# Optimization experiments

Measured on AMD Instinct MI355X. Metric: run time of the kernel, lower is better.

## Reference

```python
import jax, jax.numpy as jnp
import numpy as np

NUM_HEADS = 16
MASKED_BIAS = -10000.0


def setup_inputs() -> dict:
    key = jax.random.key(0)
    ks = jax.random.split(key, 5)
    B, S, D = 4, 2048, 1024
    return {
        "encodings": jax.random.normal(ks[0], (B, S, D), dtype=jnp.float32),
        "w_attn": jax.random.normal(ks[1], (D, 3 * D), dtype=jnp.float32) * (1.0 / np.sqrt(D)),
        "b_attn": jax.random.normal(ks[2], (3 * D,), dtype=jnp.float32) * 0.02,
        "w_proj": jax.random.normal(ks[3], (D, D), dtype=jnp.float32) * (1.0 / np.sqrt(D)),
        "b_proj": jax.random.normal(ks[4], (D,), dtype=jnp.float32) * 0.02,
    }


def reference(encodings, w_attn, b_attn, w_proj, b_proj):
    B, S, D = encodings.shape
    H = NUM_HEADS
    hs = D // H
    qkv = encodings @ w_attn + b_attn            # [B,S,3D]
    q, k, v = jnp.split(qkv, 3, axis=-1)
    # 'b s (h c) -> b h s c'
    def split_heads(x):
        return x.reshape(B, S, H, hs).transpose(0, 2, 1, 3)
    q, k, v = split_heads(q), split_heads(k), split_heads(v)
    # scores[b,h,f,t] = q[t] . k[f] / sqrt(hs)  (f=key, t=query)
    scores = jnp.einsum('bhtc,bhfc->bhft', q, k) / np.sqrt(hs).astype(jnp.float32)
    # causal: query t may attend key f iff t >= f  -> upper-tri in (f,t)
    causal = jnp.triu(jnp.ones((S, S), dtype=bool))  # [f,t]
    scores = jnp.where(causal[None, None], scores, jnp.asarray(MASKED_BIAS, scores.dtype))
    attn = jax.nn.softmax(scores, axis=-2)       # softmax over keys (f)
    ctx = jnp.einsum('bhft,bhfc->bhtc', attn, v)  # [B,H,S,hs]
    ctx = ctx.transpose(0, 2, 1, 3).reshape(B, S, D)  # 'b h s c -> b s (h c)'
    return ctx @ w_proj + b_proj
```

## Files before the change

kernel.cpp:

```cpp
#include <hip/hip_runtime.h>
#include <hip/hip_bf16.h>
#include <stdint.h>

#define NH  16
#define SEQ 2048
#define DM  1024
#define HS  64
#define NB  4

typedef __attribute__((ext_vector_type(8))) short bf16x8;
typedef __attribute__((ext_vector_type(4))) float f32x4;

__device__ __forceinline__ unsigned short f2b(float f) {
    unsigned int u = __float_as_uint(f);
    u += 0x7fffu + ((u >> 16) & 1u);
    return (unsigned short)(u >> 16);
}

__device__ __forceinline__ void gload16(const void* g, void* lds) {
    __builtin_amdgcn_global_load_lds(
        (const __attribute__((address_space(1))) unsigned int*)g,
        (__attribute__((address_space(3))) unsigned int*)lds,
        16, 0, 0);
}

__global__ void k_cvt(const float* __restrict__ in, unsigned short* __restrict__ out, int n) {
    int i = (blockIdx.x * blockDim.x + threadIdx.x) * 4;
    if (i >= n) return;
    float4 v = *(const float4*)(in + i);
    ushort4 o;
    o.x = f2b(v.x); o.y = f2b(v.y); o.z = f2b(v.z); o.w = f2b(v.w);
    *(ushort4*)(out + i) = o;
}

__global__ void k_tr(const float* __restrict__ in, unsigned short* __restrict__ out, int K, int N) {
    __shared__ float t[32][33];
    int n0 = blockIdx.x * 32, k0 = blockIdx.y * 32;
    int tx = threadIdx.x, ty = threadIdx.y;
#pragma unroll
    for (int j = 0; j < 32; j += 8)
        t[ty + j][tx] = in[(size_t)(k0 + ty + j) * N + n0 + tx];
    __syncthreads();
#pragma unroll
    for (int j = 0; j < 32; j += 8)
        out[(size_t)(n0 + ty + j) * K + k0 + tx] = f2b(t[tx][ty + j]);
}

template <int MODE>
__global__ __launch_bounds__(256, 2) void k_gemm(
    const unsigned short* __restrict__ A,
    const unsigned short* __restrict__ Bt,
    const float* __restrict__ bias,
    void* __restrict__ outp, int M, int N, int K)
{
    __shared__ unsigned short As[128 * 64];
    __shared__ unsigned short Bs[128 * 64];
    const int tid = threadIdx.x;
    const int l = tid & 63, w = tid >> 6;
    const int lg = l >> 4, li = l & 15;
    const int m0 = blockIdx.x * 128, n0 = blockIdx.y * 128;
    const int wm = (w >> 1) * 64, wn = (w & 1) * 64;

    f32x4 acc[4][4] = {};

    for (int k0 = 0; k0 < K; k0 += 64) {
#pragma unroll
        for (int i = 0; i < 4; i++) {
            int ch = i * 256 + tid;
            int row = ch >> 3, cc = ch & 7;
            int sc = cc ^ (row & 7);
            gload16(A + (size_t)(m0 + row) * K + k0 + sc * 8, &As[(i * 256 + w * 64) * 8]);
        }
#pragma unroll
        for (int i = 0; i < 4; i++) {
            int ch = i * 256 + tid;
            int row = ch >> 3, cc = ch & 7;
            int sc = cc ^ (row & 7);
            gload16(Bt + (size_t)(n0 + row) * K + k0 + sc * 8, &Bs[(i * 256 + w * 64) * 8]);
        }
        __syncthreads();
#pragma unroll
        for (int kc = 0; kc < 2; kc++) {
            bf16x8 af[4], bfr[4];
#pragma unroll
            for (int mi = 0; mi < 4; mi++) {
                int row = wm + mi * 16 + li;
                int chunk = (kc * 4 + lg) ^ (row & 7);
                af[mi] = *(const bf16x8*)&As[row * 64 + chunk * 8];
            }
#pragma unroll
            for (int ni = 0; ni < 4; ni++) {
                int row = wn + ni * 16 + li;
                int chunk = (kc * 4 + lg) ^ (row & 7);
                bfr[ni] = *(const bf16x8*)&Bs[row * 64 + chunk * 8];
            }
#pragma unroll
            for (int mi = 0; mi < 4; mi++)
#pragma unroll
                for (int ni = 0; ni < 4; ni++)
                    acc[mi][ni] = __builtin_amdgcn_mfma_f32_16x16x32_bf16(af[mi], bfr[ni], acc[mi][ni], 0, 0, 0);
        }
        __syncthreads();
    }

#pragma unroll
    for (int mi = 0; mi < 4; mi++) {
        int mrow = m0 + wm + mi * 16 + lg * 4;
#pragma unroll
        for (int ni = 0; ni < 4; ni++) {
            int col = n0 + wn + ni * 16 + li;
            float bv = bias[col];
            if (MODE == 0) {
                float* out = (float*)outp;
#pragma unroll
                for (int r = 0; r < 4; r++)
                    out[(size_t)(mrow + r) * N + col] = acc[mi][ni][r] + bv;
            } else {
                unsigned short* out = (unsigned short*)outp;
                const size_t QKV1 = (size_t)NB * NH * SEQ * HS;
                int sqkv = col >> 10;
                int d = col & 1023;
                int h = d >> 6, c = d & 63;
                float scale = (sqkv == 0) ? 0.18033688f : 1.0f;
#pragma unroll
                for (int r = 0; r < 4; r++) {
                    int m = mrow + r;
                    int bq = m >> 11, sp = m & 2047;
                    size_t off;
                    if (sqkv == 2)
                        off = 2 * QKV1 + ((size_t)(bq * NH + h) * HS + c) * SEQ + sp;
                    else
                        off = (size_t)sqkv * QKV1 + ((size_t)(bq * NH + h) * SEQ + sp) * HS + c;
                    out[off] = f2b((acc[mi][ni][r] + bv) * scale);
                }
            }
        }
    }
}

__global__ __launch_bounds__(256, 2) void k_attn(
    const unsigned short* __restrict__ qkv,
    unsigned short* __restrict__ ctx)
{
    __shared__ unsigned short Ks[2][64 * 64];
    __shared__ unsigned short Vts[2][64 * 64];
    __shared__ unsigned short Ps[4 * 32 * 64];
    const int tid = threadIdx.x;
    const int l = tid & 63, w = tid >> 6;
    const int lg = l >> 4, li = l & 15;
    const int bh = blockIdx.x;
    const int qa = blockIdx.y;
    const int qb = 15 - qa;
    const int qA0 = qa * 128, qB0 = qb * 128;
    const int na = qA0 / 64 + 2, nbt = qB0 / 64 + 2;
    const size_t hb = (size_t)bh * SEQ * HS;
    const size_t QKV1 = (size_t)NB * NH * SEQ * HS;
    const unsigned short* Qg = qkv + hb;
    const unsigned short* Kg = qkv + QKV1 + hb;
    const unsigned short* VTg = qkv + 2 * QKV1 + hb;

    bf16x8 aqA[2][2], aqB[2][2];
#pragma unroll
    for (int rt = 0; rt < 2; rt++) {
        int tA = qA0 + rt * 64 + w * 16 + li;
        aqA[rt][0] = *(const bf16x8*)(Qg + (size_t)tA * HS + lg * 8);
        aqA[rt][1] = *(const bf16x8*)(Qg + (size_t)tA * HS + 32 + lg * 8);
        int tB = qB0 + rt * 64 + w * 16 + li;
        aqB[rt][0] = *(const bf16x8*)(Qg + (size_t)tB * HS + lg * 8);
        aqB[rt][1] = *(const bf16x8*)(Qg + (size_t)tB * HS + 32 + lg * 8);
    }

    f32x4 accA[2][4] = {}, accB[2][4] = {};
    float mrA[2][4], lsA[2][4], mrB[2][4], lsB[2][4];
#pragma unroll
    for (int rt = 0; rt < 2; rt++)
#pragma unroll
        for (int r = 0; r < 4; r++) {
            mrA[rt][r] = -1e30f; lsA[rt][r] = 0.f;
            mrB[rt][r] = -1e30f; lsB[rt][r] = 0.f;
        }

    auto stage = [&](int buf, int f0) {
#pragma unroll
        for (int i = 0; i < 2; i++) {
            int ch = i * 256 + tid;
            int row = ch >> 3, cc = ch & 7;
            int sc = cc ^ (row & 7);
            gload16(Kg + (size_t)(f0 + row) * HS + sc * 8, &Ks[buf][(i * 256 + w * 64) * 8]);
        }
#pragma unroll
        for (int i = 0; i < 2; i++) {
            int ch = i * 256 + tid;
            int row = ch >> 3, cc = ch & 7;
            int sc = cc ^ (row & 7);
            gload16(VTg + (size_t)row * SEQ + f0 + sc * 8, &Vts[buf][(i * 256 + w * 64) * 8]);
        }
    };

    auto process = [&](int q0, bf16x8 (&aq)[2][2], f32x4 (&acc)[2][4],
                       float (&mr)[2][4], float (&ls)[2][4], int f0, int buf) {
#pragma unroll
        for (int rt = 0; rt < 2; rt++) {
            const int tb = q0 + rt * 64 + w * 16;
            if (f0 > tb + 15) continue;

            f32x4 sa[4] = {};
#pragma unroll
            for (int kc = 0; kc < 2; kc++)
#pragma unroll
                for (int nt = 0; nt < 4; nt++) {
                    int row = nt * 16 + li;
                    int chunk = (kc * 4 + lg) ^ (row & 7);
                    bf16x8 bk = *(const bf16x8*)&Ks[buf][row * 64 + chunk * 8];
                    sa[nt] = __builtin_amdgcn_mfma_f32_16x16x32_bf16(aq[rt][kc], bk, sa[nt], 0, 0, 0);
                }

            if (f0 + 63 > tb) {
                int trow = tb + lg * 4;
#pragma unroll
                for (int nt = 0; nt < 4; nt++) {
                    int f = f0 + nt * 16 + li;
#pragma unroll
                    for (int r = 0; r < 4; r++)
                        if (f > trow + r) sa[nt][r] = -1e30f;
                }
            }

            float pmax[4];
#pragma unroll
            for (int r = 0; r < 4; r++) {
                float rm = fmaxf(fmaxf(sa[0][r], sa[1][r]), fmaxf(sa[2][r], sa[3][r]));
                rm = fmaxf(rm, __shfl_xor(rm, 1));
                rm = fmaxf(rm, __shfl_xor(rm, 2));
                rm = fmaxf(rm, __shfl_xor(rm, 4));
                rm = fmaxf(rm, __shfl_xor(rm, 8));
                pmax[r] = rm;
            }
            bool need = false;
#pragma unroll
            for (int r = 0; r < 4; r++) need |= (pmax[r] > mr[rt][r] + 8.0f);
            if (__any(need)) {
                float corr[4];
#pragma unroll
                for (int r = 0; r < 4; r++) {
                    float mn = fmaxf(mr[rt][r], pmax[r]);
                    corr[r] = __builtin_amdgcn_exp2f(mr[rt][r] - mn);
                    mr[rt][r] = mn;
                    ls[rt][r] *= corr[r];
                }
#pragma unroll
                for (int nt = 0; nt < 4; nt++)
#pragma unroll
                    for (int r = 0; r < 4; r++)
                        acc[rt][nt][r] *= corr[r];
            }

            float rs[4] = {0.f, 0.f, 0.f, 0.f};
#pragma unroll
            for (int nt = 0; nt < 4; nt++)
#pragma unroll
                for (int r = 0; r < 4; r++) {
                    float p = __builtin_amdgcn_exp2f(sa[nt][r] - mr[rt][r]);
                    sa[nt][r] = p;
                    rs[r] += p;
                }
#pragma unroll
            for (int r = 0; r < 4; r++) {
                rs[r] += __shfl_xor(rs[r], 1);
                rs[r] += __shfl_xor(rs[r], 2);
                rs[r] += __shfl_xor(rs[r], 4);
                rs[r] += __shfl_xor(rs[r], 8);
                ls[rt][r] += rs[r];
            }

            char* PB = (char*)Ps + w * 4096 + rt * 2048;
#pragma unroll
            for (int nt = 0; nt < 4; nt++)
#pragma unroll
                for (int r = 0; r < 4; r++) {
                    int row = lg * 4 + r, f = nt * 16 + li;
                    *(unsigned short*)(PB + row * 128 + ((f * 2) ^ ((row & 7) << 4))) =
                        (unsigned short)(__float_as_uint(sa[nt][r]) >> 16);
                }

#pragma unroll
            for (int kc = 0; kc < 2; kc++) {
                int C = kc * 4 + lg;
                bf16x8 pf = *(const bf16x8*)(PB + li * 128 + ((C * 16) ^ ((li & 7) << 4)));
#pragma unroll
                for (int nt = 0; nt < 4; nt++) {
                    int c = nt * 16 + li;
                    int vch = C ^ (c & 7);
                    bf16x8 vf = *(const bf16x8*)&Vts[buf][c * 64 + vch * 8];
                    acc[rt][nt] = __builtin_amdgcn_mfma_f32_16x16x32_bf16(pf, vf, acc[rt][nt], 0, 0, 0);
                }
            }
        }
    };

    stage(0, 0);
    __syncthreads();
    for (int ft = 0; ft < nbt; ft++) {
        int buf = ft & 1;
        if (ft + 1 < nbt) stage(buf ^ 1, (ft + 1) * 64);
        process(qB0, aqB, accB, mrB, lsB, ft * 64, buf);
        if (ft < na) process(qA0, aqA, accA, mrA, lsA, ft * 64, buf);
        __syncthreads();
    }

    int b = bh >> 4, h = bh & 15;
#pragma unroll
    for (int rt = 0; rt < 2; rt++)
#pragma unroll
        for (int nt = 0; nt < 4; nt++)
#pragma unroll
            for (int r = 0; r < 4; r++) {
                int c = nt * 16 + li;
                int tB = qB0 + rt * 64 + w * 16 + lg * 4 + r;
                ctx[((size_t)(b * SEQ + tB)) * DM + h * HS + c] = f2b(accB[rt][nt][r] / lsB[rt][r]);
                int tA = qA0 + rt * 64 + w * 16 + lg * 4 + r;
                ctx[((size_t)(b * SEQ + tA)) * DM + h * HS + c] = f2b(accA[rt][nt][r] / lsA[rt][r]);
            }
}

extern "C" void kernel_launch(void* const* d_in, const int* in_sizes, int n_in,
                              void* d_out, int out_size, void* d_ws, size_t ws_size,
                              hipStream_t stream) {
    const float* enc    = (const float*)d_in[0];
    const float* w_attn = (const float*)d_in[1];
    const float* b_attn = (const float*)d_in[2];
    const float* w_proj = (const float*)d_in[3];
    const float* b_proj = (const float*)d_in[4];
    float* out = (float*)d_out;

    unsigned short* ws = (unsigned short*)d_ws;
    unsigned short* X    = ws;
    unsigned short* Wq   = ws + 8388608;
    unsigned short* Wp   = Wq + 3145728;
    unsigned short* QKV  = Wp + 1048576;
    unsigned short* CTX  = X;

    const int M = NB * SEQ;

    k_cvt<<<8192, 256, 0, stream>>>(enc, X, M * DM);
    k_tr<<<dim3(96, 32), dim3(32, 8), 0, stream>>>(w_attn, Wq, DM, 3 * DM);
    k_tr<<<dim3(32, 32), dim3(32, 8), 0, stream>>>(w_proj, Wp, DM, DM);
    k_gemm<1><<<dim3(M / 128, 24), 256, 0, stream>>>(X, Wq, b_attn, QKV, M, 3 * DM, DM);
    k_attn<<<dim3(NB * NH, 8), 256, 0, stream>>>(QKV, CTX);
    k_gemm<0><<<dim3(M / 128, 8), 256, 0, stream>>>(CTX, Wp, b_proj, out, M, DM, DM);
}
```

Measured before the change: 307.2 us.

## Raise attention occupancy, defer row-sum reductions, add MFMA priority hints

Raises k_attn launch bounds from 2 to 4 blocks per SM and halves the P scratch buffer by sharing it across the two row tiles. Row sums are kept per lane and reduced across lanes once at the end, and the row-max shuffle reduction runs only when a rescale is needed. s_setprio hints are placed around the MFMA sections in both the GEMM and the attention kernel. Together these aim to cut shuffle overhead and LDS use per block. The higher occupancy target may force register spills.

```diff
diff --git a/kernel.cpp b/kernel.cpp
--- a/kernel.cpp
+++ b/kernel.cpp
@@ -79,6 +79,7 @@
             gload16(Bt + (size_t)(n0 + row) * K + k0 + sc * 8, &Bs[(i * 256 + w * 64) * 8]);
         }
         __syncthreads();
+        __builtin_amdgcn_s_setprio(1);
 #pragma unroll
         for (int kc = 0; kc < 2; kc++) {
             bf16x8 af[4], bfr[4];
@@ -100,6 +101,7 @@
                 for (int ni = 0; ni < 4; ni++)
                     acc[mi][ni] = __builtin_amdgcn_mfma_f32_16x16x32_bf16(af[mi], bfr[ni], acc[mi][ni], 0, 0, 0);
         }
+        __builtin_amdgcn_s_setprio(0);
         __syncthreads();
     }
 
@@ -138,13 +140,13 @@
     }
 }
 
-__global__ __launch_bounds__(256, 2) void k_attn(
+__global__ __launch_bounds__(256, 4) void k_attn(
     const unsigned short* __restrict__ qkv,
     unsigned short* __restrict__ ctx)
 {
     __shared__ unsigned short Ks[2][64 * 64];
     __shared__ unsigned short Vts[2][64 * 64];
-    __shared__ unsigned short Ps[4 * 32 * 64];
+    __shared__ unsigned short Ps[4 * 16 * 64];
     const int tid = threadIdx.x;
     const int l = tid & 63, w = tid >> 6;
     const int lg = l >> 4, li = l & 15;
@@ -205,6 +207,7 @@
             if (f0 > tb + 15) continue;
 
             f32x4 sa[4] = {};
+            __builtin_amdgcn_s_setprio(1);
 #pragma unroll
             for (int kc = 0; kc < 2; kc++)
 #pragma unroll
@@ -214,6 +217,7 @@
                     bf16x8 bk = *(const bf16x8*)&Ks[buf][row * 64 + chunk * 8];
                     sa[nt] = __builtin_amdgcn_mfma_f32_16x16x32_bf16(aq[rt][kc], bk, sa[nt], 0, 0, 0);
                 }
+            __builtin_amdgcn_s_setprio(0);
 
             if (f0 + 63 > tb) {
                 int trow = tb + lg * 4;
@@ -227,53 +231,40 @@
             }
 
             float pmax[4];
+            bool need = false;
 #pragma unroll
             for (int r = 0; r < 4; r++) {
-                float rm = fmaxf(fmaxf(sa[0][r], sa[1][r]), fmaxf(sa[2][r], sa[3][r]));
-                rm = fmaxf(rm, __shfl_xor(rm, 1));
-                rm = fmaxf(rm, __shfl_xor(rm, 2));
-                rm = fmaxf(rm, __shfl_xor(rm, 4));
-                rm = fmaxf(rm, __shfl_xor(rm, 8));
-                pmax[r] = rm;
-            }
-            bool need = false;
-#pragma unroll
-            for (int r = 0; r < 4; r++) need |= (pmax[r] > mr[rt][r] + 8.0f);
+                pmax[r] = fmaxf(fmaxf(sa[0][r], sa[1][r]), fmaxf(sa[2][r], sa[3][r]));
+                need |= (pmax[r] > mr[rt][r] + 8.0f);
+            }
             if (__any(need)) {
-                float corr[4];
 #pragma unroll
                 for (int r = 0; r < 4; r++) {
-                    float mn = fmaxf(mr[rt][r], pmax[r]);
-                    corr[r] = __builtin_amdgcn_exp2f(mr[rt][r] - mn);
+                    float rm = pmax[r];
+                    rm = fmaxf(rm, __shfl_xor(rm, 1));
+                    rm = fmaxf(rm, __shfl_xor(rm, 2));
+                    rm = fmaxf(rm, __shfl_xor(rm, 4));
+                    rm = fmaxf(rm, __shfl_xor(rm, 8));
+                    float mn = fmaxf(mr[rt][r], rm);
+                    float corr = __builtin_amdgcn_exp2f(mr[rt][r] - mn);
                     mr[rt][r] = mn;
-                    ls[rt][r] *= corr[r];
-                }
-#pragma unroll
-                for (int nt = 0; nt < 4; nt++)
-#pragma unroll
-                    for (int r = 0; r < 4; r++)
-                        acc[rt][nt][r] *= corr[r];
-            }
-
-            float rs[4] = {0.f, 0.f, 0.f, 0.f};
+                    ls[rt][r] *= corr;
+#pragma unroll
+                    for (int nt = 0; nt < 4; nt++)
+                        acc[rt][nt][r] *= corr;
+                }
+            }
+
 #pragma unroll
             for (int nt = 0; nt < 4; nt++)
 #pragma unroll
                 for (int r = 0; r < 4; r++) {
                     float p = __builtin_amdgcn_exp2f(sa[nt][r] - mr[rt][r]);
                     sa[nt][r] = p;
-                    rs[r] += p;
-                }
-#pragma unroll
-            for (int r = 0; r < 4; r++) {
-                rs[r] += __shfl_xor(rs[r], 1);
-                rs[r] += __shfl_xor(rs[r], 2);
-                rs[r] += __shfl_xor(rs[r], 4);
-                rs[r] += __shfl_xor(rs[r], 8);
-                ls[rt][r] += rs[r];
-            }
-
-            char* PB = (char*)Ps + w * 4096 + rt * 2048;
+                    ls[rt][r] += p;
+                }
+
+            char* PB = (char*)Ps + w * 2048;
 #pragma unroll
             for (int nt = 0; nt < 4; nt++)
 #pragma unroll
@@ -283,6 +274,7 @@
                         (unsigned short)(__float_as_uint(sa[nt][r]) >> 16);
                 }
 
+            __builtin_amdgcn_s_setprio(1);
 #pragma unroll
             for (int kc = 0; kc < 2; kc++) {
                 int C = kc * 4 + lg;
@@ -295,6 +287,7 @@
                     acc[rt][nt] = __builtin_amdgcn_mfma_f32_16x16x32_bf16(pf, vf, acc[rt][nt], 0, 0, 0);
                 }
             }
+            __builtin_amdgcn_s_setprio(0);
         }
     };
 
@@ -312,6 +305,17 @@
 #pragma unroll
     for (int rt = 0; rt < 2; rt++)
 #pragma unroll
+        for (int r = 0; r < 4; r++) {
+            float sA = lsA[rt][r], sB = lsB[rt][r];
+            sA += __shfl_xor(sA, 1); sB += __shfl_xor(sB, 1);
+            sA += __shfl_xor(sA, 2); sB += __shfl_xor(sB, 2);
+            sA += __shfl_xor(sA, 4); sB += __shfl_xor(sB, 4);
+            sA += __shfl_xor(sA, 8); sB += __shfl_xor(sB, 8);
+            lsA[rt][r] = sA; lsB[rt][r] = sB;
+        }
+#pragma unroll
+    for (int rt = 0; rt < 2; rt++)
+#pragma unroll
         for (int nt = 0; nt < 4; nt++)
 #pragma unroll
             for (int r = 0; r < 4; r++) {
```

Measured after the change: 599.0 us. 95.0% more time.
